# Performance work log

Measured on AMD Instinct MI355X. Metric: run time of the kernel, lower is better.

The kernel has to match this reference:

```python
import jax, jax.numpy as jnp
import numpy as np

B, S, D, H, DC, HC = 2, 2048, 1024, 16, 64, 16  # batch, seq, hidden, heads, coord_dim, head_coord_dim
HD = D // H  # head_dim


def setup_inputs() -> dict:
    key = jax.random.key(0)
    ks = jax.random.split(key, 12)
    s = lambda fan_in: 1.0 / np.sqrt(fan_in)
    return {
        "hidden_states": jax.random.normal(ks[0], (B, S, D), jnp.float32),
        "coordinates": jax.random.normal(ks[1], (B, S, DC), jnp.float32),
        # weights stored [in, out] (used as x @ W + b, equivalent to torch Linear)
        "Wv": jax.random.uniform(ks[2], (D, D), jnp.float32, -s(D), s(D)),
        "bv": jax.random.uniform(ks[3], (D,), jnp.float32, -s(D), s(D)),
        "Wc": jax.random.uniform(ks[4], (DC, H * HC), jnp.float32, -s(DC), s(DC)),
        "bc": jax.random.uniform(ks[5], (H * HC,), jnp.float32, -s(DC), s(DC)),
        "Wn": jax.random.uniform(ks[6], (DC, DC), jnp.float32, -s(DC), s(DC)),
        "bn": jax.random.uniform(ks[7], (DC,), jnp.float32, -s(DC), s(DC)),
        "Wo": jax.random.uniform(ks[8], (D, D), jnp.float32, -s(D), s(D)),
        "bo": jax.random.uniform(ks[9], (D,), jnp.float32, -s(D), s(D)),
        "gamma": jax.random.normal(ks[10], (1, H, 1, 1), jnp.float32),
    }


def reference(hidden_states, coordinates, Wv, bv, Wc, bc, Wn, bn, Wo, bo, gamma):
    b, s, _ = hidden_states.shape
    # value: [B,H,S,HD]
    value = (hidden_states @ Wv + bv).reshape(b, s, H, HD).transpose(0, 2, 1, 3)
    # coord heads: [B,H,S,HC]
    z = (coordinates @ Wc + bc).reshape(b, s, H, HC).transpose(0, 2, 1, 3)
    z_sq = jnp.sum(z * z, axis=-1, keepdims=True)  # [B,H,S,1]
    sq_dist = z_sq + jnp.swapaxes(z_sq, -1, -2) - 2.0 * jnp.einsum("bhsc,bhtc->bhst", z, z)
    sq_dist = jnp.maximum(sq_dist, 0.0)
    g = jax.nn.softplus(gamma)  # [1,H,1,1]
    attn = jax.nn.softmax(-g * sq_dist, axis=-1)  # [B,H,S,S]
    out = jnp.einsum("bhst,bhtd->bhsd", attn, value)
    out = out.transpose(0, 2, 1, 3).reshape(b, s, D)
    updated_hidden = out @ Wo + bo
    updated_coords = coordinates @ Wn + bn
    return (updated_hidden, updated_coords)
```

## Files before the change

kernel.cpp:

```cpp
#include <hip/hip_runtime.h>
#include <hip/hip_bf16.h>

typedef short bf16x8 __attribute__((ext_vector_type(8)));
typedef float f32x4 __attribute__((ext_vector_type(4)));
typedef float f32x16 __attribute__((ext_vector_type(16)));
typedef unsigned short u16;
typedef unsigned int u32;

__device__ __forceinline__ u16 f2b(float f) {
  __hip_bfloat16 h = __float2bfloat16(f);
  return *reinterpret_cast<u16*>(&h);
}

#define MFMA16(a, b, c) __builtin_amdgcn_mfma_f32_16x16x32_bf16((a), (b), (c), 0, 0, 0)
#define MFMA32(a, b, c) __builtin_amdgcn_mfma_f32_32x32x16_bf16((a), (b), (c), 0, 0, 0)


__global__ __launch_bounds__(256) void k_prep2(const float* __restrict__ hs,
                                               u16* __restrict__ HSb,
                                               const float* __restrict__ Wv,
                                               u16* __restrict__ WvT,
                                               const float* __restrict__ Wo,
                                               u16* __restrict__ WoT) {
  __shared__ float t[64][65];
  int tid = threadIdx.x, blk = blockIdx.x;
  if (blk < 4096) {
    int i = (blk * 256 + tid) * 4;
    float4 v = *reinterpret_cast<const float4*>(hs + i);
    ushort4 o;
    o.x = f2b(v.x); o.y = f2b(v.y); o.z = f2b(v.z); o.w = f2b(v.w);
    *reinterpret_cast<ushort4*>(HSb + i) = o;
    return;
  }
  const float* W = (blk < 4352) ? Wv : Wo;
  u16* WT = (blk < 4352) ? WvT : WoT;
  int bid = (blk < 4352) ? blk - 4096 : blk - 4352;
  int r0 = (bid & 15) << 6, c0 = (bid >> 4) << 6;
#pragma unroll
  for (int rep = 0; rep < 4; ++rep) {
    int e = tid + rep * 256;
    int r = e >> 4, c4 = (e & 15) << 2;
    float4 v = *reinterpret_cast<const float4*>(W + (size_t)(r0 + r) * 1024 + c0 + c4);
    t[r][c4] = v.x; t[r][c4 + 1] = v.y; t[r][c4 + 2] = v.z; t[r][c4 + 3] = v.w;
  }
  __syncthreads();
#pragma unroll
  for (int rep = 0; rep < 4; ++rep) {
    int e = tid + rep * 256;
    int c = e >> 4, r4 = (e & 15) << 2;
    ushort4 o;
    o.x = f2b(t[r4][c]); o.y = f2b(t[r4 + 1][c]);
    o.z = f2b(t[r4 + 2][c]); o.w = f2b(t[r4 + 3][c]);
    *reinterpret_cast<ushort4*>(WT + (size_t)(c0 + c) * 1024 + r0 + r4) = o;
  }
}

__global__ void k_z(const float* __restrict__ C, const float* __restrict__ Wc,
                    const float* __restrict__ bc, const float* __restrict__ gamma,
                    u16* __restrict__ Z, u16* __restrict__ Zg, u32* __restrict__ zghl) {
  int gid = blockIdx.x * 256 + threadIdx.x;
  int bs = gid >> 4, h = gid & 15;
  float gm = gamma[h];
  float g = (gm > 15.f) ? gm : log1pf(__expf(gm));
  float g2 = g * 1.4426950408889634f;
  float tg2 = 2.f * g2;
  const float* crow = C + (size_t)bs * 64;
  float acc[16];
#pragma unroll
  for (int c = 0; c < 16; ++c) acc[c] = bc[h * 16 + c];
  for (int k = 0; k < 64; ++k) {
    float cv = crow[k];
    const float* wr = Wc + (size_t)k * 256 + h * 16;
#pragma unroll
    for (int c = 0; c < 16; ++c) acc[c] = fmaf(cv, wr[c], acc[c]);
  }
  float sq = 0.f;
  u16 tz[16], tg[16];
#pragma unroll
  for (int c = 0; c < 16; ++c) {
    sq += acc[c] * acc[c];
    tz[c] = f2b(acc[c]);
    tg[c] = f2b(tg2 * acc[c]);
  }
  float x = -g2 * sq;
  u32 xu = __float_as_uint(x);
  float xh = __uint_as_float(xu & 0xFFFF0000u);
  u32 packed = (xu >> 16) | ((u32)f2b(x - xh) << 16);
  int b = bs >> 11, s = bs & 2047;
  int bh = (b << 4) + h;
  size_t ro = (((size_t)bh << 11) + s) * 16;
  *reinterpret_cast<uint4*>(Z + ro) = *reinterpret_cast<uint4*>(tz);
  *reinterpret_cast<uint4*>(Z + ro + 8) = *reinterpret_cast<uint4*>(tz + 8);
  *reinterpret_cast<uint4*>(Zg + ro) = *reinterpret_cast<uint4*>(tg);
  *reinterpret_cast<uint4*>(Zg + ro + 8) = *reinterpret_cast<uint4*>(tg + 8);
  zghl[((size_t)bh << 11) + s] = packed;
}

__global__ void k_coords(const float* __restrict__ C, const float* __restrict__ Wn,
                         const float* __restrict__ bn, float* __restrict__ out) {
  int gid = blockIdx.x * 256 + threadIdx.x;
  int bs = gid >> 6, c = gid & 63;
  const float* crow = C + (size_t)bs * 64;
  float acc = bn[c];
#pragma unroll 8
  for (int k = 0; k < 64; ++k) acc = fmaf(crow[k], Wn[k * 64 + c], acc);
  out[gid] = acc;
}

template <int OUTM>
__global__ __launch_bounds__(512, 4) void k_gemm(const u16* __restrict__ A,
                                                 const u16* __restrict__ BT,
                                                 const float* __restrict__ bias,
                                                 void* __restrict__ Cout,
                                                 int M, int N, int K) {
  __shared__ u16 As[2][128 * 64];
  __shared__ u16 Bs[2][64 * 64];
  int wg = ((blockIdx.x & 7) << 6) + (blockIdx.x >> 3);
  int bm = wg >> 4, bn = wg & 15;
  int tid = threadIdx.x, lane = tid & 63, w = tid >> 6;
  int wm = w >> 1, wn = w & 1;
  int l15 = lane & 15, lg = lane >> 4;
  int lr = lane >> 3;
  int swc = (lane & 7) ^ lr;

  f32x4 acc[2][2];
#pragma unroll
  for (int mi = 0; mi < 2; ++mi)
#pragma unroll
    for (int ni = 0; ni < 2; ++ni) acc[mi][ni] = (f32x4){0.f, 0.f, 0.f, 0.f};

  const u16* Abase = A + (size_t)(bm * 128 + w * 8 + lr) * K + swc * 8;
  const u16* Bbase = BT + (size_t)(bn * 64 + w * 8 + lr) * K + swc * 8;
  int rsw = l15 & 7;

#define GSTAGE(BUF, KK)                                                             \
  do {                                                                              \
    __builtin_amdgcn_global_load_lds(                                               \
        (const __attribute__((address_space(1))) u32*)(Abase + (KK)),               \
        (__attribute__((address_space(3))) u32*)&As[(BUF)][(w * 8) * 64], 16, 0, 0);\
    __builtin_amdgcn_global_load_lds(                                               \
        (const __attribute__((address_space(1))) u32*)(Abase + (size_t)64 * K + (KK)),\
        (__attribute__((address_space(3))) u32*)&As[(BUF)][(64 + w * 8) * 64], 16, 0, 0);\
    __builtin_amdgcn_global_load_lds(                                               \
        (const __attribute__((address_space(1))) u32*)(Bbase + (KK)),               \
        (__attribute__((address_space(3))) u32*)&Bs[(BUF)][(w * 8) * 64], 16, 0, 0);\
  } while (0)

  const int nk = K >> 6;
  GSTAGE(0, 0);
  for (int it = 0; it < nk; ++it) {
    int cur = it & 1;
    if (it + 1 < nk) {
      GSTAGE(cur ^ 1, (it + 1) * 64);
      asm volatile("s_waitcnt vmcnt(3)" ::: "memory");
    } else {
      asm volatile("s_waitcnt vmcnt(0)" ::: "memory");
    }
    __builtin_amdgcn_sched_barrier(0);
    __builtin_amdgcn_s_barrier();
#pragma unroll
    for (int kk = 0; kk < 2; ++kk) {
      int ch = (kk * 4 + lg) ^ rsw;
      bf16x8 af[2], bfr[2];
#pragma unroll
      for (int mi = 0; mi < 2; ++mi)
        af[mi] = *reinterpret_cast<const bf16x8*>(&As[cur][(wm * 32 + mi * 16 + l15) * 64 + ch * 8]);
#pragma unroll
      for (int ni = 0; ni < 2; ++ni)
        bfr[ni] = *reinterpret_cast<const bf16x8*>(&Bs[cur][(wn * 32 + ni * 16 + l15) * 64 + ch * 8]);
#pragma unroll
      for (int mi = 0; mi < 2; ++mi)
#pragma unroll
        for (int ni = 0; ni < 2; ++ni)
          acc[mi][ni] = MFMA16(af[mi], bfr[ni], acc[mi][ni]);
    }
    __builtin_amdgcn_sched_barrier(0);
    __builtin_amdgcn_s_barrier();
  }
#undef GSTAGE

#pragma unroll
  for (int mi = 0; mi < 2; ++mi) {
#pragma unroll
    for (int ni = 0; ni < 2; ++ni) {
      int col = bn * 64 + wn * 32 + ni * 16 + l15;
      float bv = bias[col];
      if (OUTM == 0) {
#pragma unroll
        for (int j = 0; j < 4; ++j) {
          int row = bm * 128 + wm * 32 + mi * 16 + lg * 4 + j;
          reinterpret_cast<float*>(Cout)[(size_t)row * N + col] = acc[mi][ni][j] + bv;
        }
      } else {
        int row0 = bm * 128 + wm * 32 + mi * 16 + lg * 4;
        int b = row0 >> 11, tg = (row0 >> 4) & 127;
        int hi_ = lg >> 1, jb = (lg & 1) << 2;
        int h = col >> 6, hd = col & 63, dh = hd >> 5, lv = hd & 31;
        size_t addr = ((((size_t)(b * 16 + h) * 128 + tg) * 2 + dh) << 9) +
                      ((hi_ * 32 + lv) << 3) + jb;
        ushort4 o;
        o.x = f2b(acc[mi][ni][0] + bv); o.y = f2b(acc[mi][ni][1] + bv);
        o.z = f2b(acc[mi][ni][2] + bv); o.w = f2b(acc[mi][ni][3] + bv);
        *reinterpret_cast<ushort4*>(reinterpret_cast<u16*>(Cout) + addr) = o;
      }
    }
  }
}

__global__ __launch_bounds__(256, 2) void k_attn(const u16* __restrict__ Z,
                                                 const u16* __restrict__ Zg,
                                                 const u32* __restrict__ zghl,
                                                 const u16* __restrict__ VF,
                                                 u16* __restrict__ O) {
  __shared__ __align__(16) char smem[33792];
  float* psqf = reinterpret_cast<float*>(smem + 32768);

  int tid = threadIdx.x, lane = tid & 63, w = tid >> 6;
  int l31 = lane & 31, hi = lane >> 5;
  int hi4 = hi << 2, hi8 = hi << 3;
  int th = w & 1, qh = w >> 1, th32 = th << 5;
  int wg = ((blockIdx.x & 7) << 6) + (blockIdx.x >> 3);
  int bh = wg >> 4, qt = wg & 15;
  int q0 = qt << 7;
  int h = bh & 15, bb = bh >> 4;

  const u16* Zb = Z + ((size_t)bh << 11) * 16;
  const u16* Zgb = Zg + ((size_t)bh << 11) * 16;
  const u32* ghl = zghl + ((size_t)bh << 11);
  const u16* VFb = VF + ((size_t)bh << 17);

  int qx0 = (qh << 6) + l31;
  int qx1 = qx0 + 32;

  bf16x8 zq2_0 = *reinterpret_cast<const bf16x8*>(Zgb + (size_t)(q0 + qx0) * 16 + hi8);
  bf16x8 zq2_1 = *reinterpret_cast<const bf16x8*>(Zgb + (size_t)(q0 + qx1) * 16 + hi8);

  u32 gq0 = ghl[q0 + qx0], gq1 = ghl[q0 + qx1];
  uint4 ab0 = {0x3F803F80u, gq0, 0u, 0u};
  uint4 ab1 = {0x3F803F80u, gq1, 0u, 0u};
  if (hi) { ab0.x = 0u; ab0.y = 0u; ab1.x = 0u; ab1.y = 0u; }
  bf16x8 aug_b0 = *reinterpret_cast<bf16x8*>(&ab0);
  bf16x8 aug_b1 = *reinterpret_cast<bf16x8*>(&ab1);

  uint4 aqu = {0u, 0x3F803F80u, 0u, 0u};
  if (hi) aqu.y = 0u;
  bf16x8 aug_q = *reinterpret_cast<bf16x8*>(&aqu);
  f32x16 qpart0 = MFMA32(aug_q, aug_b0, (f32x16){});
  f32x16 qpart1 = MFMA32(aug_q, aug_b1, (f32x16){});

  const u16* zap = Zb + (size_t)(th32 + l31) * 16 + hi8;
  const u32* xtp = ghl + th32 + l31;
  const u16* vwp = VFb + ((size_t)th << 11) + ((size_t)lane << 3);

  f32x16 oacc00 = {}, oacc01 = {}, oacc10 = {}, oacc11 = {};
  f32x4 ps0 = {}, ps1 = {};

  int swz = (l31 ^ (l31 >> 2)) & 3;
  char* pbase = smem + (w << 12) + l31 * 64;

  bf16x8 zA_c = *reinterpret_cast<const bf16x8*>(zap);
  u32 zhl_c = xtp[0];
  bf16x8 vc0 = *reinterpret_cast<const bf16x8*>(vwp);
  bf16x8 vc1 = *reinterpret_cast<const bf16x8*>(vwp + 512);
  bf16x8 vc2 = *reinterpret_cast<const bf16x8*>(vwp + 1024);
  bf16x8 vc3 = *reinterpret_cast<const bf16x8*>(vwp + 1536);

#pragma unroll 2
  for (int tt = 0; tt < 32; ++tt) {
    const int t0 = tt << 6;
    bf16x8 zA_n = zA_c, vn0 = vc0, vn1 = vc1, vn2 = vc2, vn3 = vc3;
    u32 zhl_n = zhl_c;
    if (tt < 31) {
      const u16* vtb = vwp + ((tt + 1) << 12);
      zA_n = *reinterpret_cast<const bf16x8*>(zap + (size_t)(t0 + 64) * 16);
      zhl_n = xtp[t0 + 64];
      vn0 = *reinterpret_cast<const bf16x8*>(vtb);
      vn1 = *reinterpret_cast<const bf16x8*>(vtb + 512);
      vn2 = *reinterpret_cast<const bf16x8*>(vtb + 1024);
      vn3 = *reinterpret_cast<const bf16x8*>(vtb + 1536);
    }

    uint4 aau = {hi ? 0u : zhl_c, 0u, 0u, 0u};
    bf16x8 aug_a = *reinterpret_cast<bf16x8*>(&aau);

    f32x16 sc0 = MFMA32(aug_a, aug_b0, qpart0);
    sc0 = MFMA32(zA_c, zq2_0, sc0);
    f32x16 sc1 = MFMA32(aug_a, aug_b1, qpart1);
    sc1 = MFMA32(zA_c, zq2_1, sc1);

    char* pb = pbase + ((tt & 1) << 14);
#pragma unroll
    for (int g = 0; g < 4; ++g) {
      int cb = ((g ^ swz) << 4) + (hi << 3);
      {
        float e0 = fminf(sc0[g * 4 + 0], 0.f), e1 = fminf(sc0[g * 4 + 1], 0.f);
        float e2 = fminf(sc0[g * 4 + 2], 0.f), e3 = fminf(sc0[g * 4 + 3], 0.f);
        float p0 = __builtin_amdgcn_exp2f(e0), p1 = __builtin_amdgcn_exp2f(e1);
        float p2 = __builtin_amdgcn_exp2f(e2), p3 = __builtin_amdgcn_exp2f(e3);
        ps0[0] += p0; ps0[1] += p1; ps0[2] += p2; ps0[3] += p3;
        u32 pk0, pk1;
        asm("v_cvt_pk_bf16_f32 %0, %1, %2" : "=v"(pk0) : "v"(p0), "v"(p1));
        asm("v_cvt_pk_bf16_f32 %0, %1, %2" : "=v"(pk1) : "v"(p2), "v"(p3));
        uint2 pkv = {pk0, pk1};
        *reinterpret_cast<uint2*>(pb + cb) = pkv;
      }
      {
        float e0 = fminf(sc1[g * 4 + 0], 0.f), e1 = fminf(sc1[g * 4 + 1], 0.f);
        float e2 = fminf(sc1[g * 4 + 2], 0.f), e3 = fminf(sc1[g * 4 + 3], 0.f);
        float p0 = __builtin_amdgcn_exp2f(e0), p1 = __builtin_amdgcn_exp2f(e1);
        float p2 = __builtin_amdgcn_exp2f(e2), p3 = __builtin_amdgcn_exp2f(e3);
        ps1[0] += p0; ps1[1] += p1; ps1[2] += p2; ps1[3] += p3;
        u32 pk0, pk1;
        asm("v_cvt_pk_bf16_f32 %0, %1, %2" : "=v"(pk0) : "v"(p0), "v"(p1));
        asm("v_cvt_pk_bf16_f32 %0, %1, %2" : "=v"(pk1) : "v"(p2), "v"(p3));
        uint2 pkv = {pk0, pk1};
        *reinterpret_cast<uint2*>(pb + 2048 + cb) = pkv;
      }
    }

    int c0b = (((0 * 2 + hi) ^ swz) << 4);
    int c1b = (((1 * 2 + hi) ^ swz) << 4);
    bf16x8 pa00 = *reinterpret_cast<const bf16x8*>(pb + c0b);
    bf16x8 pa01 = *reinterpret_cast<const bf16x8*>(pb + c1b);
    bf16x8 pa10 = *reinterpret_cast<const bf16x8*>(pb + 2048 + c0b);
    bf16x8 pa11 = *reinterpret_cast<const bf16x8*>(pb + 2048 + c1b);

    __builtin_amdgcn_s_setprio(1);
    oacc00 = MFMA32(pa00, vc0, oacc00);
    oacc01 = MFMA32(pa00, vc1, oacc01);
    oacc10 = MFMA32(pa10, vc0, oacc10);
    oacc11 = MFMA32(pa10, vc1, oacc11);
    oacc00 = MFMA32(pa01, vc2, oacc00);
    oacc01 = MFMA32(pa01, vc3, oacc01);
    oacc10 = MFMA32(pa11, vc2, oacc10);
    oacc11 = MFMA32(pa11, vc3, oacc11);
    __builtin_amdgcn_s_setprio(0);

    zA_c = zA_n; zhl_c = zhl_n;
    vc0 = vn0; vc1 = vn1; vc2 = vn2; vc3 = vn3;
  }

  float psum0 = (ps0[0] + ps0[1]) + (ps0[2] + ps0[3]);
  float psum1 = (ps1[0] + ps1[1]) + (ps1[2] + ps1[3]);
  psum0 += __shfl_xor(psum0, 32, 64);
  psum1 += __shfl_xor(psum1, 32, 64);

  __syncthreads();
  if (th == 1) {
    char* dst = smem + ((w >> 1) << 14) + lane * 16;
#pragma unroll
    for (int r = 0; r < 4; ++r) {
      *reinterpret_cast<f32x4*>(dst + (0 + r) * 1024) =
          (f32x4){oacc00[r * 4], oacc00[r * 4 + 1], oacc00[r * 4 + 2], oacc00[r * 4 + 3]};
      *reinterpret_cast<f32x4*>(dst + (4 + r) * 1024) =
          (f32x4){oacc01[r * 4], oacc01[r * 4 + 1], oacc01[r * 4 + 2], oacc01[r * 4 + 3]};
      *reinterpret_cast<f32x4*>(dst + (8 + r) * 1024) =
          (f32x4){oacc10[r * 4], oacc10[r * 4 + 1], oacc10[r * 4 + 2], oacc10[r * 4 + 3]};
      *reinterpret_cast<f32x4*>(dst + (12 + r) * 1024) =
          (f32x4){oacc11[r * 4], oacc11[r * 4 + 1], oacc11[r * 4 + 2], oacc11[r * 4 + 3]};
    }
  }
  if (lane < 32) {
    psqf[(w * 2 + 0) * 32 + l31] = psum0;
    psqf[(w * 2 + 1) * 32 + l31] = psum1;
  }
  __syncthreads();
  if (th == 0) {
    const char* src = smem + ((w >> 1) << 14) + lane * 16;
#pragma unroll
    for (int r = 0; r < 4; ++r) {
      f32x4 v0 = *reinterpret_cast<const f32x4*>(src + (0 + r) * 1024);
      f32x4 v1 = *reinterpret_cast<const f32x4*>(src + (4 + r) * 1024);
      f32x4 v2 = *reinterpret_cast<const f32x4*>(src + (8 + r) * 1024);
      f32x4 v3 = *reinterpret_cast<const f32x4*>(src + (12 + r) * 1024);
#pragma unroll
      for (int j = 0; j < 4; ++j) {
        oacc00[r * 4 + j] += v0[j];
        oacc01[r * 4 + j] += v1[j];
        oacc10[r * 4 + j] += v2[j];
        oacc11[r * 4 + j] += v3[j];
      }
    }
#pragma unroll
    for (int qbk = 0; qbk < 2; ++qbk) {
#pragma unroll
      for (int g = 0; g < 4; ++g) {
        f32x4 a = *reinterpret_cast<const f32x4*>(&psqf[(w * 2 + qbk) * 32 + (g << 3) + hi4]);
        f32x4 b2 = *reinterpret_cast<const f32x4*>(&psqf[((w + 1) * 2 + qbk) * 32 + (g << 3) + hi4]);
#pragma unroll
        for (int j = 0; j < 4; ++j) {
          float inv = __builtin_amdgcn_rcpf(a[j] + b2[j]);
          int qrow = (g << 3) + hi4 + j;
          int srow = q0 + (qh << 6) + (qbk << 5) + qrow;
          u16* orow = O + ((size_t)(bb * 2048 + srow) << 10) + h * 64 + l31;
          float v0 = (qbk ? oacc10[g * 4 + j] : oacc00[g * 4 + j]);
          float v1 = (qbk ? oacc11[g * 4 + j] : oacc01[g * 4 + j]);
          orow[0] = f2b(v0 * inv);
          orow[32] = f2b(v1 * inv);
        }
      }
    }
  }
}

extern "C" void kernel_launch(void* const* d_in, const int* in_sizes, int n_in,
                              void* d_out, int out_size, void* d_ws, size_t ws_size,
                              hipStream_t stream) {
  const float* hs     = (const float*)d_in[0];
  const float* coords = (const float*)d_in[1];
  const float* Wv     = (const float*)d_in[2];
  const float* bv     = (const float*)d_in[3];
  const float* Wc     = (const float*)d_in[4];
  const float* bc     = (const float*)d_in[5];
  const float* Wn     = (const float*)d_in[6];
  const float* bn     = (const float*)d_in[7];
  const float* Wo     = (const float*)d_in[8];
  const float* bo     = (const float*)d_in[9];
  const float* gamma  = (const float*)d_in[10];
  float* out_h = (float*)d_out;
  float* out_c = out_h + 4194304;

  char* ws = (char*)d_ws;
  u16*   HSb  = (u16*)(ws + 0);
  u16*   O    = (u16*)(ws + 0);
  u16*   WvT  = (u16*)(ws + 8388608);
  u16*   WoT  = (u16*)(ws + 10485760);
  u16*   Zw   = (u16*)(ws + 12582912);
  u16*   Zgw  = (u16*)(ws + 14680064);
  u32*   zghl = (u32*)(ws + 16777216);
  u16*   VFw  = (u16*)(ws + 17039360);

  k_prep2<<<4608, 256, 0, stream>>>(hs, HSb, Wv, WvT, Wo, WoT);
  k_z<<<256, 256, 0, stream>>>(coords, Wc, bc, gamma, Zw, Zgw, zghl);
  k_gemm<1><<<512, 512, 0, stream>>>(HSb, WvT, bv, VFw, 4096, 1024, 1024);
  k_attn<<<512, 256, 0, stream>>>(Zw, Zgw, zghl, VFw, O);
  k_gemm<0><<<512, 512, 0, stream>>>(O, WoT, bo, out_h, 4096, 1024, 1024);
  k_coords<<<1024, 256, 0, stream>>>(coords, Wn, bn, out_c);
}
```

Measured before the change: 107.2 us.

## Halve attention query tile to 64 rows, doubling blocks and occupancy

The attention kernel now processes 64 query rows per block instead of 128, so each wave handles one 32-row query sub-block instead of two. The grid doubles to 1024 blocks, shared memory halves, and launch bounds allow four blocks per CU, aiming for more parallelism and latency hiding. In exchange, every K/V tile is loaded twice as often, and each wave has less independent MFMA work to interleave per iteration.

```diff
diff --git a/kernel.cpp b/kernel.cpp
--- a/kernel.cpp
+++ b/kernel.cpp
@@ -207,21 +207,21 @@
   }
 }
 
-__global__ __launch_bounds__(256, 2) void k_attn(const u16* __restrict__ Z,
+__global__ __launch_bounds__(256, 4) void k_attn(const u16* __restrict__ Z,
                                                  const u16* __restrict__ Zg,
                                                  const u32* __restrict__ zghl,
                                                  const u16* __restrict__ VF,
                                                  u16* __restrict__ O) {
-  __shared__ __align__(16) char smem[33792];
-  float* psqf = reinterpret_cast<float*>(smem + 32768);
+  __shared__ __align__(16) char smem[16896];
+  float* psqf = reinterpret_cast<float*>(smem + 16384);
 
   int tid = threadIdx.x, lane = tid & 63, w = tid >> 6;
   int l31 = lane & 31, hi = lane >> 5;
   int hi4 = hi << 2, hi8 = hi << 3;
   int th = w & 1, qh = w >> 1, th32 = th << 5;
-  int wg = ((blockIdx.x & 7) << 6) + (blockIdx.x >> 3);
-  int bh = wg >> 4, qt = wg & 15;
-  int q0 = qt << 7;
+  int wg = ((blockIdx.x & 7) << 7) + (blockIdx.x >> 3);
+  int bh = wg >> 5, qt = wg & 31;
+  int q0 = qt << 6;
   int h = bh & 15, bb = bh >> 4;
 
   const u16* Zb = Z + ((size_t)bh << 11) * 16;
@@ -229,34 +229,29 @@
   const u32* ghl = zghl + ((size_t)bh << 11);
   const u16* VFb = VF + ((size_t)bh << 17);
 
-  int qx0 = (qh << 6) + l31;
-  int qx1 = qx0 + 32;
-
-  bf16x8 zq2_0 = *reinterpret_cast<const bf16x8*>(Zgb + (size_t)(q0 + qx0) * 16 + hi8);
-  bf16x8 zq2_1 = *reinterpret_cast<const bf16x8*>(Zgb + (size_t)(q0 + qx1) * 16 + hi8);
-
-  u32 gq0 = ghl[q0 + qx0], gq1 = ghl[q0 + qx1];
-  uint4 ab0 = {0x3F803F80u, gq0, 0u, 0u};
-  uint4 ab1 = {0x3F803F80u, gq1, 0u, 0u};
-  if (hi) { ab0.x = 0u; ab0.y = 0u; ab1.x = 0u; ab1.y = 0u; }
-  bf16x8 aug_b0 = *reinterpret_cast<bf16x8*>(&ab0);
-  bf16x8 aug_b1 = *reinterpret_cast<bf16x8*>(&ab1);
+  int qx = (qh << 5) + l31;
+
+  bf16x8 zq2 = *reinterpret_cast<const bf16x8*>(Zgb + (size_t)(q0 + qx) * 16 + hi8);
+
+  u32 gq = ghl[q0 + qx];
+  uint4 ab0 = {0x3F803F80u, gq, 0u, 0u};
+  if (hi) { ab0.x = 0u; ab0.y = 0u; }
+  bf16x8 aug_b = *reinterpret_cast<bf16x8*>(&ab0);
 
   uint4 aqu = {0u, 0x3F803F80u, 0u, 0u};
   if (hi) aqu.y = 0u;
   bf16x8 aug_q = *reinterpret_cast<bf16x8*>(&aqu);
-  f32x16 qpart0 = MFMA32(aug_q, aug_b0, (f32x16){});
-  f32x16 qpart1 = MFMA32(aug_q, aug_b1, (f32x16){});
+  f32x16 qpart = MFMA32(aug_q, aug_b, (f32x16){});
 
   const u16* zap = Zb + (size_t)(th32 + l31) * 16 + hi8;
   const u32* xtp = ghl + th32 + l31;
   const u16* vwp = VFb + ((size_t)th << 11) + ((size_t)lane << 3);
 
-  f32x16 oacc00 = {}, oacc01 = {}, oacc10 = {}, oacc11 = {};
-  f32x4 ps0 = {}, ps1 = {};
+  f32x16 oacc0 = {}, oacc1 = {};
+  f32x4 ps = {};
 
   int swz = (l31 ^ (l31 >> 2)) & 3;
-  char* pbase = smem + (w << 12) + l31 * 64;
+  char* pbase = smem + (w << 11) + l31 * 64;
 
   bf16x8 zA_c = *reinterpret_cast<const bf16x8*>(zap);
   u32 zhl_c = xtp[0];
@@ -283,121 +278,81 @@
     uint4 aau = {hi ? 0u : zhl_c, 0u, 0u, 0u};
     bf16x8 aug_a = *reinterpret_cast<bf16x8*>(&aau);
 
-    f32x16 sc0 = MFMA32(aug_a, aug_b0, qpart0);
-    sc0 = MFMA32(zA_c, zq2_0, sc0);
-    f32x16 sc1 = MFMA32(aug_a, aug_b1, qpart1);
-    sc1 = MFMA32(zA_c, zq2_1, sc1);
-
-    char* pb = pbase + ((tt & 1) << 14);
+    f32x16 sc = MFMA32(aug_a, aug_b, qpart);
+    sc = MFMA32(zA_c, zq2, sc);
+
+    char* pb = pbase + ((tt & 1) << 13);
 #pragma unroll
     for (int g = 0; g < 4; ++g) {
       int cb = ((g ^ swz) << 4) + (hi << 3);
-      {
-        float e0 = fminf(sc0[g * 4 + 0], 0.f), e1 = fminf(sc0[g * 4 + 1], 0.f);
-        float e2 = fminf(sc0[g * 4 + 2], 0.f), e3 = fminf(sc0[g * 4 + 3], 0.f);
-        float p0 = __builtin_amdgcn_exp2f(e0), p1 = __builtin_amdgcn_exp2f(e1);
-        float p2 = __builtin_amdgcn_exp2f(e2), p3 = __builtin_amdgcn_exp2f(e3);
-        ps0[0] += p0; ps0[1] += p1; ps0[2] += p2; ps0[3] += p3;
-        u32 pk0, pk1;
-        asm("v_cvt_pk_bf16_f32 %0, %1, %2" : "=v"(pk0) : "v"(p0), "v"(p1));
-        asm("v_cvt_pk_bf16_f32 %0, %1, %2" : "=v"(pk1) : "v"(p2), "v"(p3));
-        uint2 pkv = {pk0, pk1};
-        *reinterpret_cast<uint2*>(pb + cb) = pkv;
-      }
-      {
-        float e0 = fminf(sc1[g * 4 + 0], 0.f), e1 = fminf(sc1[g * 4 + 1], 0.f);
-        float e2 = fminf(sc1[g * 4 + 2], 0.f), e3 = fminf(sc1[g * 4 + 3], 0.f);
-        float p0 = __builtin_amdgcn_exp2f(e0), p1 = __builtin_amdgcn_exp2f(e1);
-        float p2 = __builtin_amdgcn_exp2f(e2), p3 = __builtin_amdgcn_exp2f(e3);
-        ps1[0] += p0; ps1[1] += p1; ps1[2] += p2; ps1[3] += p3;
-        u32 pk0, pk1;
-        asm("v_cvt_pk_bf16_f32 %0, %1, %2" : "=v"(pk0) : "v"(p0), "v"(p1));
-        asm("v_cvt_pk_bf16_f32 %0, %1, %2" : "=v"(pk1) : "v"(p2), "v"(p3));
-        uint2 pkv = {pk0, pk1};
-        *reinterpret_cast<uint2*>(pb + 2048 + cb) = pkv;
-      }
+      float e0 = fminf(sc[g * 4 + 0], 0.f), e1 = fminf(sc[g * 4 + 1], 0.f);
+      float e2 = fminf(sc[g * 4 + 2], 0.f), e3 = fminf(sc[g * 4 + 3], 0.f);
+      float p0 = __builtin_amdgcn_exp2f(e0), p1 = __builtin_amdgcn_exp2f(e1);
+      float p2 = __builtin_amdgcn_exp2f(e2), p3 = __builtin_amdgcn_exp2f(e3);
+      ps[0] += p0; ps[1] += p1; ps[2] += p2; ps[3] += p3;
+      u32 pk0, pk1;
+      asm("v_cvt_pk_bf16_f32 %0, %1, %2" : "=v"(pk0) : "v"(p0), "v"(p1));
+      asm("v_cvt_pk_bf16_f32 %0, %1, %2" : "=v"(pk1) : "v"(p2), "v"(p3));
+      uint2 pkv = {pk0, pk1};
+      *reinterpret_cast<uint2*>(pb + cb) = pkv;
     }
 
     int c0b = (((0 * 2 + hi) ^ swz) << 4);
     int c1b = (((1 * 2 + hi) ^ swz) << 4);
-    bf16x8 pa00 = *reinterpret_cast<const bf16x8*>(pb + c0b);
-    bf16x8 pa01 = *reinterpret_cast<const bf16x8*>(pb + c1b);
-    bf16x8 pa10 = *reinterpret_cast<const bf16x8*>(pb + 2048 + c0b);
-    bf16x8 pa11 = *reinterpret_cast<const bf16x8*>(pb + 2048 + c1b);
+    bf16x8 pa0 = *reinterpret_cast<const bf16x8*>(pb + c0b);
+    bf16x8 pa1 = *reinterpret_cast<const bf16x8*>(pb + c1b);
 
     __builtin_amdgcn_s_setprio(1);
-    oacc00 = MFMA32(pa00, vc0, oacc00);
-    oacc01 = MFMA32(pa00, vc1, oacc01);
-    oacc10 = MFMA32(pa10, vc0, oacc10);
-    oacc11 = MFMA32(pa10, vc1, oacc11);
-    oacc00 = MFMA32(pa01, vc2, oacc00);
-    oacc01 = MFMA32(pa01, vc3, oacc01);
-    oacc10 = MFMA32(pa11, vc2, oacc10);
-    oacc11 = MFMA32(pa11, vc3, oacc11);
+    oacc0 = MFMA32(pa0, vc0, oacc0);
+    oacc1 = MFMA32(pa0, vc1, oacc1);
+    oacc0 = MFMA32(pa1, vc2, oacc0);
+    oacc1 = MFMA32(pa1, vc3, oacc1);
     __builtin_amdgcn_s_setprio(0);
 
     zA_c = zA_n; zhl_c = zhl_n;
     vc0 = vn0; vc1 = vn1; vc2 = vn2; vc3 = vn3;
   }
 
-  float psum0 = (ps0[0] + ps0[1]) + (ps0[2] + ps0[3]);
-  float psum1 = (ps1[0] + ps1[1]) + (ps1[2] + ps1[3]);
-  psum0 += __shfl_xor(psum0, 32, 64);
-  psum1 += __shfl_xor(psum1, 32, 64);
+  float psum = (ps[0] + ps[1]) + (ps[2] + ps[3]);
+  psum += __shfl_xor(psum, 32, 64);
 
   __syncthreads();
   if (th == 1) {
-    char* dst = smem + ((w >> 1) << 14) + lane * 16;
+    char* dst = smem + ((w >> 1) << 13) + lane * 16;
 #pragma unroll
     for (int r = 0; r < 4; ++r) {
       *reinterpret_cast<f32x4*>(dst + (0 + r) * 1024) =
-          (f32x4){oacc00[r * 4], oacc00[r * 4 + 1], oacc00[r * 4 + 2], oacc00[r * 4 + 3]};
+          (f32x4){oacc0[r * 4], oacc0[r * 4 + 1], oacc0[r * 4 + 2], oacc0[r * 4 + 3]};
       *reinterpret_cast<f32x4*>(dst + (4 + r) * 1024) =
-          (f32x4){oacc01[r * 4], oacc01[r * 4 + 1], oacc01[r * 4 + 2], oacc01[r * 4 + 3]};
-      *reinterpret_cast<f32x4*>(dst + (8 + r) * 1024) =
-          (f32x4){oacc10[r * 4], oacc10[r * 4 + 1], oacc10[r * 4 + 2], oacc10[r * 4 + 3]};
-      *reinterpret_cast<f32x4*>(dst + (12 + r) * 1024) =
-          (f32x4){oacc11[r * 4], oacc11[r * 4 + 1], oacc11[r * 4 + 2], oacc11[r * 4 + 3]};
-    }
-  }
-  if (lane < 32) {
-    psqf[(w * 2 + 0) * 32 + l31] = psum0;
-    psqf[(w * 2 + 1) * 32 + l31] = psum1;
-  }
+          (f32x4){oacc1[r * 4], oacc1[r * 4 + 1], oacc1[r * 4 + 2], oacc1[r * 4 + 3]};
+    }
+  }
+  if (lane < 32) psqf[w * 32 + l31] = psum;
   __syncthreads();
   if (th == 0) {
-    const char* src = smem + ((w >> 1) << 14) + lane * 16;
+    const char* src = smem + ((w >> 1) << 13) + lane * 16;
 #pragma unroll
     for (int r = 0; r < 4; ++r) {
       f32x4 v0 = *reinterpret_cast<const f32x4*>(src + (0 + r) * 1024);
       f32x4 v1 = *reinterpret_cast<const f32x4*>(src + (4 + r) * 1024);
-      f32x4 v2 = *reinterpret_cast<const f32x4*>(src + (8 + r) * 1024);
-      f32x4 v3 = *reinterpret_cast<const f32x4*>(src + (12 + r) * 1024);
 #pragma unroll
       for (int j = 0; j < 4; ++j) {
-        oacc00[r * 4 + j] += v0[j];
-        oacc01[r * 4 + j] += v1[j];
-        oacc10[r * 4 + j] += v2[j];
-        oacc11[r * 4 + j] += v3[j];
+        oacc0[r * 4 + j] += v0[j];
+        oacc1[r * 4 + j] += v1[j];
       }
     }
 #pragma unroll
-    for (int qbk = 0; qbk < 2; ++qbk) {
-#pragma unroll
-      for (int g = 0; g < 4; ++g) {
-        f32x4 a = *reinterpret_cast<const f32x4*>(&psqf[(w * 2 + qbk) * 32 + (g << 3) + hi4]);
-        f32x4 b2 = *reinterpret_cast<const f32x4*>(&psqf[((w + 1) * 2 + qbk) * 32 + (g << 3) + hi4]);
-#pragma unroll
-        for (int j = 0; j < 4; ++j) {
-          float inv = __builtin_amdgcn_rcpf(a[j] + b2[j]);
-          int qrow = (g << 3) + hi4 + j;
-          int srow = q0 + (qh << 6) + (qbk << 5) + qrow;
-          u16* orow = O + ((size_t)(bb * 2048 + srow) << 10) + h * 64 + l31;
-          float v0 = (qbk ? oacc10[g * 4 + j] : oacc00[g * 4 + j]);
-          float v1 = (qbk ? oacc11[g * 4 + j] : oacc01[g * 4 + j]);
-          orow[0] = f2b(v0 * inv);
-          orow[32] = f2b(v1 * inv);
-        }
+    for (int g = 0; g < 4; ++g) {
+      f32x4 a = *reinterpret_cast<const f32x4*>(&psqf[w * 32 + (g << 3) + hi4]);
+      f32x4 b2 = *reinterpret_cast<const f32x4*>(&psqf[(w + 1) * 32 + (g << 3) + hi4]);
+#pragma unroll
+      for (int j = 0; j < 4; ++j) {
+        float inv = __builtin_amdgcn_rcpf(a[j] + b2[j]);
+        int qrow = (g << 3) + hi4 + j;
+        int srow = q0 + (qh << 5) + qrow;
+        u16* orow = O + ((size_t)(bb * 2048 + srow) << 10) + h * 64 + l31;
+        orow[0] = f2b(oacc0[g * 4 + j] * inv);
+        orow[32] = f2b(oacc1[g * 4 + j] * inv);
       }
     }
   }
@@ -433,7 +388,7 @@
   k_prep2<<<4608, 256, 0, stream>>>(hs, HSb, Wv, WvT, Wo, WoT);
   k_z<<<256, 256, 0, stream>>>(coords, Wc, bc, gamma, Zw, Zgw, zghl);
   k_gemm<1><<<512, 512, 0, stream>>>(HSb, WvT, bv, VFw, 4096, 1024, 1024);
-  k_attn<<<512, 256, 0, stream>>>(Zw, Zgw, zghl, VFw, O);
+  k_attn<<<1024, 256, 0, stream>>>(Zw, Zgw, zghl, VFw, O);
   k_gemm<0><<<512, 512, 0, stream>>>(O, WoT, bo, out_h, 4096, 1024, 1024);
   k_coords<<<1024, 256, 0, stream>>>(coords, Wn, bn, out_c);
 }
```

After: 242.4 us. 2.26x slower.
